# Kernel tuning notes

Hardware: AMD Instinct MI355X
Metric: run time of the kernel (lower is better)

The kernel has to match this reference:

```python
import jax, jax.numpy as jnp
import numpy as np
from jax import lax

NUM_CLASSES = 80
CONF_THRE = 0.01   # testconf in source
NMS_THRE = 0.2     # nmsthresh in source
N = 8400           # YOLOX anchors at 640x640: 80^2+40^2+20^2
IMG = 640.0


def setup_inputs() -> dict:
    key = jax.random.key(0)
    pred = jax.random.uniform(key, (N, 5 + NUM_CLASSES), dtype=jnp.float32)
    # scale cx,cy,w,h to pixel units so boxes are realistic
    pred = pred.at[:, :4].multiply(IMG)
    return {"prediction": pred}


def _pairwise_iou(boxes):
    # boxes: [N,4] in x1,y1,x2,y2
    area = (boxes[:, 2] - boxes[:, 0]) * (boxes[:, 3] - boxes[:, 1])  # [N]
    lt = jnp.maximum(boxes[:, None, :2], boxes[None, :, :2])  # [N,N,2]
    rb = jnp.minimum(boxes[:, None, 2:], boxes[None, :, 2:])  # [N,N,2]
    wh = jnp.clip(rb - lt, 0.0)
    inter = wh[..., 0] * wh[..., 1]
    return inter / (area[:, None] + area[None, :] - inter + 1e-9)


def reference(prediction):
    # ---- box corner decode (cx,cy,w,h -> x1,y1,x2,y2) ----
    cx, cy, w, h = prediction[:, 0], prediction[:, 1], prediction[:, 2], prediction[:, 3]
    boxes = jnp.stack([cx - w / 2, cy - h / 2, cx + w / 2, cy + h / 2], axis=1)

    # ---- per-class max ----
    cls_scores = prediction[:, 5:5 + NUM_CLASSES]
    class_conf = jnp.max(cls_scores, axis=1, keepdims=True)            # [N,1]
    class_pred = jnp.argmax(cls_scores, axis=1).astype(prediction.dtype)[:, None]

    obj = prediction[:, 4]
    valid = obj >= CONF_THRE                                            # conf mask

    # detections = [x1,y1,x2,y2, obj_conf, class_conf, class_pred]  -> [N,7]
    det = jnp.concatenate([boxes, obj[:, None], class_conf, class_pred], axis=1)

    # ---- class-agnostic greedy NMS on obj score (fixed-shape version) ----
    scores = jnp.where(valid, obj, -1.0)
    order = jnp.argsort(-scores)
    det_s = det[order]
    boxes_s = boxes[order]
    valid_s = valid[order]

    iou = _pairwise_iou(boxes_s)  # [N,N] ~282MB, dominant traffic
    idx = jnp.arange(N)

    def step(keep, inp):
        i, row, v = inp
        alive = keep[i] & v                      # only a kept valid box suppresses
        supp = alive & (row > NMS_THRE) & (idx > i)
        return keep & ~supp, None

    keep0 = jnp.ones((N,), dtype=bool)
    keep, _ = lax.scan(step, keep0, (idx, iou, valid_s))
    keep = keep & valid_s

    # suppressed / below-conf rows are zeroed (torch returns a ragged subset;
    # here we return the score-sorted, mask-zeroed fixed-shape equivalent)
    out = det_s * keep[:, None].astype(det_s.dtype)
    return out
```

## Files before the change

### kernel.cpp

```cpp
#include <hip/hip_runtime.h>
#include <stdint.h>

#define N_BOX 8400
#define NCLS 80
#define PSTRIDE 85
#define NW 132
#define NTILE 8778
#define ZROWI N_BOX
#define CONF_T 0.01f
#define NMS_T 0.2f

typedef unsigned long long u64;

#define OFF_DET     0
#define OFF_DIAGT   0
#define OFF_SUP1    67584
#define OFF_SUP2    135168
#define OFF_SUP3    202752
#define OFF_KEYS    268800
#define OFF_DETS    336000
#define OFF_BOXESS  604800
#define OFF_MASK    739200
#define OFF_KEEPW   9610656
#define OFF_VCNT    9611712

__device__ __forceinline__ unsigned fmap_desc(float f) {
    unsigned u = __float_as_uint(f);
    unsigned m = (u & 0x80000000u) ? ~u : (u | 0x80000000u);
    return ~m;
}

__device__ __forceinline__ u64 readlane64(u64 v, int lane) {
    unsigned lo = (unsigned)__builtin_amdgcn_readlane((int)(unsigned)v, lane);
    unsigned hi = (unsigned)__builtin_amdgcn_readlane((int)(unsigned)(v >> 32), lane);
    return ((u64)hi << 32) | lo;
}

__device__ __forceinline__ u64 shfl_xor64(u64 v, int m) {
    int lo = __shfl_xor((int)(unsigned)v, m);
    int hi = __shfl_xor((int)(unsigned)(v >> 32), m);
    return ((u64)(unsigned)hi << 32) | (unsigned)lo;
}

__device__ __forceinline__ u64 bittranspose64(u64 x, int lane) {
    const u64 P0 = 0x5555555555555555ull, P1 = 0x3333333333333333ull,
              P2 = 0x0F0F0F0F0F0F0F0Full, P3 = 0x00FF00FF00FF00FFull,
              P4 = 0x0000FFFF0000FFFFull, P5 = 0x00000000FFFFFFFFull;
#define TSTEP(s, p) do {                                                 \
        u64 y = shfl_xor64(x, s);                                        \
        x = (lane & (s)) ? ((x & ~(p)) | ((y & ~(p)) >> (s)))            \
                         : ((x & (p))  | ((y & (p))  << (s)));           \
    } while (0)
    TSTEP(1, P0); TSTEP(2, P1); TSTEP(4, P2);
    TSTEP(8, P3); TSTEP(16, P4); TSTEP(32, P5);
#undef TSTEP
    return x;
}

__device__ __forceinline__ u64 wmask(int w, int V) {
    int nb = V - (w << 6);
    if (nb <= 0) return 0ull;
    if (nb >= 64) return ~0ull;
    return (1ull << nb) - 1ull;
}

__device__ __forceinline__ void step_barrier() {
    asm volatile("s_waitcnt lgkmcnt(0)" ::: "memory");
    __builtin_amdgcn_s_barrier();
    asm volatile("" ::: "memory");
}

__global__ __launch_bounds__(256) void prep_k(const float* __restrict__ pred,
                                              float* __restrict__ det,
                                              unsigned* __restrict__ keys,
                                              u64* __restrict__ mask) {
    if (blockIdx.x == 0 && threadIdx.x < NW)
        mask[(size_t)ZROWI * NW + threadIdx.x] = 0ull;
    int gt = blockIdx.x * 256 + threadIdx.x;
    int i = gt >> 2, q = gt & 3;
    if (i >= N_BOX) return;
    const float* p = pred + (size_t)i * PSTRIDE;
    int cbase = q * 20;
    float best = p[5 + cbase];
    int arg = cbase;
    for (int c = 1; c < 20; ++c) {
        float v = p[5 + cbase + c];
        if (v > best) { best = v; arg = cbase + c; }
    }
    for (int d = 1; d < 4; d <<= 1) {
        float ob = __shfl_xor(best, d);
        int   oa = __shfl_xor(arg, d);
        if (ob > best || (ob == best && oa < arg)) { best = ob; arg = oa; }
    }
    if (q == 0) {
        float cx = p[0], cy = p[1], w = p[2], h = p[3], obj = p[4];
        float hw = __fmul_rn(w, 0.5f), hh = __fmul_rn(h, 0.5f);
        float x1 = __fsub_rn(cx, hw), y1 = __fsub_rn(cy, hh);
        float x2 = __fadd_rn(cx, hw), y2 = __fadd_rn(cy, hh);
        bool valid = (obj >= CONF_T);
        float score = valid ? obj : -1.0f;
        keys[i] = fmap_desc(score);
        float4* dr = (float4*)(det + (size_t)i * 8);
        dr[0] = make_float4(x1, y1, x2, y2);
        dr[1] = make_float4(obj, best, (float)arg, 0.0f);
    }
}

__global__ __launch_bounds__(256) void rank_k(const unsigned* __restrict__ keys,
                                              const float* __restrict__ det,
                                              float4* __restrict__ det_s,
                                              float4* __restrict__ boxes_s,
                                              int* __restrict__ vcount) {
    int t = threadIdx.x;
    int i = blockIdx.x * 32 + (t & 31);
    int s = t >> 5;
    unsigned my = (i < N_BOX) ? keys[i] : 0xFFFFFFFFu;
    int cnt = 0, cv = 0;
    int j0 = s * 1056;
    int jend = (s == 7) ? N_BOX : (j0 + 1056);
    for (int j = j0; j < jend; j += 4) {
        uint4 k4 = *(const uint4*)(keys + j);
        cnt += (k4.x < my) + (k4.y < my) + (k4.z < my) + (k4.w < my);
        cnt += (k4.x == my && j     < i) + (k4.y == my && j + 1 < i)
             + (k4.z == my && j + 2 < i) + (k4.w == my && j + 3 < i);
        cv  += ((int)k4.x >= 0) + ((int)k4.y >= 0) + ((int)k4.z >= 0) + ((int)k4.w >= 0);
    }
    __shared__ int sc[256], sv[256];
    sc[t] = cnt; sv[t] = cv;
    __syncthreads();
    if (t < 32) {
        int r = sc[t] + sc[t + 32] + sc[t + 64] + sc[t + 96]
              + sc[t + 128] + sc[t + 160] + sc[t + 192] + sc[t + 224];
        if (i < N_BOX) {
            const float4* dr = (const float4*)(det + (size_t)i * 8);
            float4 b0 = dr[0], b1 = dr[1];
            det_s[(size_t)r * 2]     = b0;
            det_s[(size_t)r * 2 + 1] = b1;
            boxes_s[r] = b0;
        }
        if (blockIdx.x == 0 && t == 0) {
            *vcount = sv[0] + sv[32] + sv[64] + sv[96]
                    + sv[128] + sv[160] + sv[192] + sv[224];
        }
    }
}

__global__ __launch_bounds__(64) void mask_k(const float4* __restrict__ boxes_s,
                                             u64* __restrict__ mask,
                                             u64* __restrict__ diagT,
                                             u64* __restrict__ sup1,
                                             u64* __restrict__ sup2,
                                             u64* __restrict__ sup3) {
    int tt = blockIdx.x, lane = threadIdx.x;
    int rb = (int)((2.0f * NW + 1.0f
                    - sqrtf((2.0f * NW + 1.0f) * (2.0f * NW + 1.0f) - 8.0f * (float)tt)) * 0.5f);
    while (rb > 0 && rb * NW - rb * (rb - 1) / 2 > tt) rb--;
    while ((rb + 1) * NW - (rb + 1) * rb / 2 <= tt) rb++;
    int cb = rb + (tt - (rb * NW - rb * (rb - 1) / 2));

    __shared__ float4 cB[64];
    __shared__ float  cA[64];
    int c0 = cb * 64 + lane;
    float4 b = (c0 < N_BOX) ? boxes_s[c0] : make_float4(0.f, 0.f, 0.f, 0.f);
    cB[lane] = b;
    cA[lane] = __fmul_rn(__fsub_rn(b.z, b.x), __fsub_rn(b.w, b.y));
    __syncthreads();
    int r = rb * 64 + lane;
    bool inb = (r < N_BOX);
    float4 rx = boxes_s[inb ? r : (N_BOX - 1)];
    float ra = __fmul_rn(__fsub_rn(rx.z, rx.x), __fsub_rn(rx.w, rx.y));
    u64 bits = 0ull;
    int cbase = cb * 64;
    for (int j = 0; j < 64; ++j) {
        int c = cbase + j;
        if (c >= N_BOX || c <= r) continue;
        float4 cx4 = cB[j];
        float ltx = fmaxf(rx.x, cx4.x), lty = fmaxf(rx.y, cx4.y);
        float rbx = fminf(rx.z, cx4.z), rby = fminf(rx.w, cx4.w);
        float wx = fmaxf(__fsub_rn(rbx, ltx), 0.0f);
        float wy = fmaxf(__fsub_rn(rby, lty), 0.0f);
        float inter = __fmul_rn(wx, wy);
        float denom = __fadd_rn(__fsub_rn(__fadd_rn(ra, cA[j]), inter), 1e-9f);
        float iou = __fdiv_rn(inter, denom);
        if (iou > NMS_T) bits |= (1ull << j);
    }
    if (inb) mask[(size_t)r * NW + cb] = bits;
    int d = cb - rb;
    if (d <= 3) {
        u64 tb = bittranspose64(bits, lane);
        size_t idx = (size_t)cb * 64 + lane;
        if (d == 0)      diagT[idx] = tb;
        else if (d == 1) sup1[idx]  = tb;
        else if (d == 2) sup2[idx]  = tb;
        else             sup3[idx]  = tb;
    }
}

__global__ __launch_bounds__(192, 1) void scan_k(const u64* __restrict__ mask,
                                                 const u64* __restrict__ diagT,
                                                 const u64* __restrict__ sup1,
                                                 const u64* __restrict__ sup2,
                                                 const u64* __restrict__ sup3,
                                                 const int* __restrict__ vcount,
                                                 u64* __restrict__ keepw) {
    __shared__ u64 remvP1[NW + 2];
    __shared__ u64 remvP2[NW + 2];
    __shared__ u64 Lbuf[NW];
    int tid = threadIdx.x, lane = tid & 63, wv = tid >> 6;
    int V = *vcount;
    for (int i = tid; i < NW + 2; i += 192) { remvP1[i] = 0ull; remvP2[i] = 0ull; }
    __syncthreads();

    if (wv == 0) {
        u64 A1 = 0ull, A2 = 0ull, A3 = 0ull;
        u64 d0P, s1P, s2P, s3P, d0Q, s1Q, s2Q, s3Q;
#define TL(S, kk) do {                                                   \
        int t_ = (kk) < NW ? (kk) : (NW - 1);                            \
        size_t ix_ = (size_t)t_ * 64 + lane;                             \
        d0##S = diagT[ix_]; s1##S = sup1[ix_];                           \
        s2##S = sup2[ix_];  s3##S = sup3[ix_];                           \
    } while (0)
#define STEP0(kk, S) do {                                                \
        int k_ = (kk);                                                   \
        u64 cur_ = remvP1[k_] | remvP2[k_];                              \
        cur_ |= __ballot((s1##S & A1) != 0ull);                          \
        cur_ |= __ballot((s2##S & A2) != 0ull);                          \
        cur_ |= __ballot((s3##S & A3) != 0ull);                          \
        u64 m_ = wmask(k_, V);                                           \
        u64 ns_ = (~cur_) & m_;                                          \
        u64 L_ = 0ull;                                                   \
        while (ns_) {                                                    \
            int b_ = __builtin_ctzll(ns_);                               \
            L_ |= 1ull << b_;                                            \
            u64 sup_ = __ballot((int)((d0##S >> b_) & 1ull));            \
            ns_ &= ~sup_;                                                \
            ns_ &= ~(1ull << b_);                                        \
        }                                                                \
        if (lane == 0) { Lbuf[k_] = L_; keepw[k_] = L_; }                \
        A3 = A2; A2 = A1; A1 = L_;                                       \
        TL(S, k_ + 2);                                                   \
        step_barrier();                                                  \
    } while (0)
        TL(P, 0);
        TL(Q, 1);
        for (int c = 0; c < NW; c += 2) {
            STEP0(c + 0, P);
            STEP0(c + 1, Q);
        }
#undef STEP0
#undef TL
    } else {
        int half = wv - 1;
        u64* myP = half ? remvP2 : remvP1;
        int tw = (lane < 4) ? (128 + lane) : 131;
        u64 Ra = 0ull, Rb = 0ull, Rc = 0ull;
        u64 Pa0=0,Pa1=0,Pa2=0,Pa3=0, Pb0=0,Pb1=0,Pb2=0,Pb3=0, Pc0=0,Pc1=0,Pc2=0,Pc3=0;
        u64 Qa0=0,Qa1=0,Qa2=0,Qa3=0, Qb0=0,Qb1=0,Qb2=0,Qb3=0, Qc0=0,Qc1=0,Qc2=0,Qc3=0;

#define CONS(S) do {                                                     \
        Ra |= (S##a0 | S##a1) | (S##a2 | S##a3);                         \
        Rb |= (S##b0 | S##b1) | (S##b2 | S##b3);                         \
        Rc |= (S##c0 | S##c1) | (S##c2 | S##c3);                         \
    } while (0)

#define LROW(S, i) do {                                                  \
        size_t ri_ = rem_ ? (size_t)(rbase_ + __builtin_ctz(rem_))       \
                          : (size_t)ZROWI;                               \
        rem_ &= rem_ - 1u;                                               \
        const u64* rp_ = mask + ri_ * NW;                                \
        ulonglong2 v_ = *(const ulonglong2*)(rp_ + 2 * lane);            \
        S##a##i = v_.x; S##b##i = v_.y; S##c##i = rp_[tw];               \
    } while (0)

#define STEP1(jj, S) do {                                                \
        int j_ = (jj);                                                   \
        CONS(S);                                  \
        int w_ = j_ + 1;                                                 \
        u64 rw_ = (w_ < 128) ? ((w_ & 1) ? Rb : Ra) : Rc;                \
        int sl_ = (w_ < 128) ? (w_ >> 1) : (w_ - 128);                   \
        u64 pv_ = readlane64(rw_, sl_);                                  \
        if (lane == 0) myP[w_] = pv_;                                    \
        u64 Lfull_ = (j_ >= 1) ? Lbuf[j_ - 1] : 0ull;                    \
        unsigned rem_ = half ? (unsigned)(Lfull_ >> 32)                  \
                             : (unsigned)Lfull_;                         \
        int rbase_ = ((j_ - 1) << 6) + 32 * half;                        \
        LROW(S, 0); LROW(S, 1); LROW(S, 2); LROW(S, 3);                  \
        while (rem_) {                              \
            u64 xa_ = 0, xb_ = 0, xc_ = 0;                               \
            for (int q_ = 0; q_ < 8; ++q_) {                             \
                size_t ri_ = rem_ ? (size_t)(rbase_ + __builtin_ctz(rem_)) \
                                  : (size_t)ZROWI;                       \
                rem_ &= rem_ - 1u;                                       \
                const u64* rp_ = mask + ri_ * NW;                        \
                ulonglong2 v_ = *(const ulonglong2*)(rp_ + 2 * lane);    \
                xa_ |= v_.x; xb_ |= v_.y; xc_ |= rp_[tw];                \
            }                                                            \
            Ra |= xa_; Rb |= xb_; Rc |= xc_;                             \
        }                                                                \
        step_barrier();                                                  \
    } while (0)

        for (int c = 0; c < NW; c += 2) {
            STEP1(c + 0, P);
            STEP1(c + 1, Q);
        }
#undef STEP1
#undef LROW
#undef CONS
    }
}

__global__ __launch_bounds__(256) void out_k(const float* __restrict__ det_s,
                                             const u64* __restrict__ keepw,
                                             float* __restrict__ out) {
    int e = blockIdx.x * 256 + threadIdx.x;
    if (e >= N_BOX * 7) return;
    int r = e / 7, c = e - r * 7;
    bool k = (keepw[r >> 6] >> (r & 63)) & 1ull;
    out[e] = k ? det_s[r * 8 + c] : 0.0f;
}

extern "C" void kernel_launch(void* const* d_in, const int* in_sizes, int n_in,
                              void* d_out, int out_size, void* d_ws, size_t ws_size,
                              hipStream_t stream) {
    const float* pred = (const float*)d_in[0];
    char* ws = (char*)d_ws;
    float*    det     = (float*)   (ws + OFF_DET);
    u64*      diagT   = (u64*)     (ws + OFF_DIAGT);
    u64*      sup1    = (u64*)     (ws + OFF_SUP1);
    u64*      sup2    = (u64*)     (ws + OFF_SUP2);
    u64*      sup3    = (u64*)     (ws + OFF_SUP3);
    unsigned* keys    = (unsigned*)(ws + OFF_KEYS);
    float*    det_s   = (float*)   (ws + OFF_DETS);
    float4*   boxes_s = (float4*)  (ws + OFF_BOXESS);
    u64*      mask    = (u64*)     (ws + OFF_MASK);
    u64*      keepw   = (u64*)     (ws + OFF_KEEPW);
    int*      vcount  = (int*)     (ws + OFF_VCNT);

    prep_k<<<132, 256, 0, stream>>>(pred, det, keys, mask);
    rank_k<<<264, 256, 0, stream>>>(keys, det, (float4*)det_s, boxes_s, vcount);
    mask_k<<<NTILE, 64, 0, stream>>>(boxes_s, mask, diagT, sup1, sup2, sup3);
    scan_k<<<1, 192, 0, stream>>>(mask, diagT, sup1, sup2, sup3, vcount, keepw);
    out_k <<<(N_BOX * 7 + 255) / 256, 256, 0, stream>>>(det_s, keepw, (float*)d_out);
}
```

Baseline: 155.0 us.

## Fuse output write into scan, pack index into sort keys, batch mask tiles

The output-zeroing kernel is folded into the single-block scan kernel. It now reads the keep bits from shared memory instead of a global keepw buffer, which saves one launch and a global round trip. Sort keys become 64-bit, with the original index packed in the low bits, so the rank kernel no longer needs a separate tie-break comparison. The mask kernel now processes four 64x64 tiles per 256-thread block instead of one tile per 64-thread block. The risk is that the fused output loop runs on only 192 threads of a single block, which serialises about 58.8k stores that were previously spread across many blocks.

```diff
diff --git a/kernel.cpp b/kernel.cpp
--- a/kernel.cpp
+++ b/kernel.cpp
@@ -21,7 +21,6 @@
 #define OFF_DETS    336000
 #define OFF_BOXESS  604800
 #define OFF_MASK    739200
-#define OFF_KEEPW   9610656
 #define OFF_VCNT    9611712
 
 __device__ __forceinline__ unsigned fmap_desc(float f) {
@@ -72,7 +71,7 @@
 
 __global__ __launch_bounds__(256) void prep_k(const float* __restrict__ pred,
                                               float* __restrict__ det,
-                                              unsigned* __restrict__ keys,
+                                              u64* __restrict__ keys,
                                               u64* __restrict__ mask) {
     if (blockIdx.x == 0 && threadIdx.x < NW)
         mask[(size_t)ZROWI * NW + threadIdx.x] = 0ull;
@@ -99,14 +98,14 @@
         float x2 = __fadd_rn(cx, hw), y2 = __fadd_rn(cy, hh);
         bool valid = (obj >= CONF_T);
         float score = valid ? obj : -1.0f;
-        keys[i] = fmap_desc(score);
+        keys[i] = ((u64)fmap_desc(score) << 32) | (unsigned)i;
         float4* dr = (float4*)(det + (size_t)i * 8);
         dr[0] = make_float4(x1, y1, x2, y2);
         dr[1] = make_float4(obj, best, (float)arg, 0.0f);
     }
 }
 
-__global__ __launch_bounds__(256) void rank_k(const unsigned* __restrict__ keys,
+__global__ __launch_bounds__(256) void rank_k(const u64* __restrict__ keys,
                                               const float* __restrict__ det,
                                               float4* __restrict__ det_s,
                                               float4* __restrict__ boxes_s,
@@ -114,16 +113,13 @@
     int t = threadIdx.x;
     int i = blockIdx.x * 32 + (t & 31);
     int s = t >> 5;
-    unsigned my = (i < N_BOX) ? keys[i] : 0xFFFFFFFFu;
+    u64 my = (i < N_BOX) ? keys[i] : ~0ull;
     int cnt = 0, cv = 0;
-    int j0 = s * 1056;
-    int jend = (s == 7) ? N_BOX : (j0 + 1056);
-    for (int j = j0; j < jend; j += 4) {
-        uint4 k4 = *(const uint4*)(keys + j);
-        cnt += (k4.x < my) + (k4.y < my) + (k4.z < my) + (k4.w < my);
-        cnt += (k4.x == my && j     < i) + (k4.y == my && j + 1 < i)
-             + (k4.z == my && j + 2 < i) + (k4.w == my && j + 3 < i);
-        cv  += ((int)k4.x >= 0) + ((int)k4.y >= 0) + ((int)k4.z >= 0) + ((int)k4.w >= 0);
+    int j0 = s * 1050, j1 = j0 + 1050;
+    for (int j = j0; j < j1; j += 2) {
+        ulonglong2 kk = *(const ulonglong2*)(keys + j);
+        cnt += (kk.x < my) + (kk.y < my);
+        cv  += ((long long)kk.x >= 0) + ((long long)kk.y >= 0);
     }
     __shared__ int sc[256], sv[256];
     sc[t] = cnt; sv[t] = cv;
@@ -145,26 +141,31 @@
     }
 }
 
-__global__ __launch_bounds__(64) void mask_k(const float4* __restrict__ boxes_s,
-                                             u64* __restrict__ mask,
-                                             u64* __restrict__ diagT,
-                                             u64* __restrict__ sup1,
-                                             u64* __restrict__ sup2,
-                                             u64* __restrict__ sup3) {
-    int tt = blockIdx.x, lane = threadIdx.x;
-    int rb = (int)((2.0f * NW + 1.0f
+__global__ __launch_bounds__(256) void mask_k(const float4* __restrict__ boxes_s,
+                                              u64* __restrict__ mask,
+                                              u64* __restrict__ diagT,
+                                              u64* __restrict__ sup1,
+                                              u64* __restrict__ sup2,
+                                              u64* __restrict__ sup3) {
+    int sub = threadIdx.x >> 6, lane = threadIdx.x & 63;
+    int tt = blockIdx.x * 4 + sub;
+    bool tv = (tt < NTILE);
+    __shared__ float4 cB[4][64];
+    __shared__ float  cA[4][64];
+    int rb = 0, cb = 0;
+    if (tv) {
+        rb = (int)((2.0f * NW + 1.0f
                     - sqrtf((2.0f * NW + 1.0f) * (2.0f * NW + 1.0f) - 8.0f * (float)tt)) * 0.5f);
-    while (rb > 0 && rb * NW - rb * (rb - 1) / 2 > tt) rb--;
-    while ((rb + 1) * NW - (rb + 1) * rb / 2 <= tt) rb++;
-    int cb = rb + (tt - (rb * NW - rb * (rb - 1) / 2));
-
-    __shared__ float4 cB[64];
-    __shared__ float  cA[64];
-    int c0 = cb * 64 + lane;
-    float4 b = (c0 < N_BOX) ? boxes_s[c0] : make_float4(0.f, 0.f, 0.f, 0.f);
-    cB[lane] = b;
-    cA[lane] = __fmul_rn(__fsub_rn(b.z, b.x), __fsub_rn(b.w, b.y));
+        while (rb > 0 && rb * NW - rb * (rb - 1) / 2 > tt) rb--;
+        while ((rb + 1) * NW - (rb + 1) * rb / 2 <= tt) rb++;
+        cb = rb + (tt - (rb * NW - rb * (rb - 1) / 2));
+        int c0 = cb * 64 + lane;
+        float4 b = (c0 < N_BOX) ? boxes_s[c0] : make_float4(0.f, 0.f, 0.f, 0.f);
+        cB[sub][lane] = b;
+        cA[sub][lane] = __fmul_rn(__fsub_rn(b.z, b.x), __fsub_rn(b.w, b.y));
+    }
     __syncthreads();
+    if (!tv) return;
     int r = rb * 64 + lane;
     bool inb = (r < N_BOX);
     float4 rx = boxes_s[inb ? r : (N_BOX - 1)];
@@ -174,13 +175,13 @@
     for (int j = 0; j < 64; ++j) {
         int c = cbase + j;
         if (c >= N_BOX || c <= r) continue;
-        float4 cx4 = cB[j];
+        float4 cx4 = cB[sub][j];
         float ltx = fmaxf(rx.x, cx4.x), lty = fmaxf(rx.y, cx4.y);
         float rbx = fminf(rx.z, cx4.z), rby = fminf(rx.w, cx4.w);
         float wx = fmaxf(__fsub_rn(rbx, ltx), 0.0f);
         float wy = fmaxf(__fsub_rn(rby, lty), 0.0f);
         float inter = __fmul_rn(wx, wy);
-        float denom = __fadd_rn(__fsub_rn(__fadd_rn(ra, cA[j]), inter), 1e-9f);
+        float denom = __fadd_rn(__fsub_rn(__fadd_rn(ra, cA[sub][j]), inter), 1e-9f);
         float iou = __fdiv_rn(inter, denom);
         if (iou > NMS_T) bits |= (1ull << j);
     }
@@ -202,7 +203,8 @@
                                                  const u64* __restrict__ sup2,
                                                  const u64* __restrict__ sup3,
                                                  const int* __restrict__ vcount,
-                                                 u64* __restrict__ keepw) {
+                                                 const float* __restrict__ det_s,
+                                                 float* __restrict__ out) {
     __shared__ u64 remvP1[NW + 2];
     __shared__ u64 remvP2[NW + 2];
     __shared__ u64 Lbuf[NW];
@@ -236,7 +238,7 @@
             ns_ &= ~sup_;                                                \
             ns_ &= ~(1ull << b_);                                        \
         }                                                                \
-        if (lane == 0) { Lbuf[k_] = L_; keepw[k_] = L_; }                \
+        if (lane == 0) Lbuf[k_] = L_;                                    \
         A3 = A2; A2 = A1; A1 = L_;                                       \
         TL(S, k_ + 2);                                                   \
         step_barrier();                                                  \
@@ -308,16 +310,13 @@
 #undef LROW
 #undef CONS
     }
-}
-
-__global__ __launch_bounds__(256) void out_k(const float* __restrict__ det_s,
-                                             const u64* __restrict__ keepw,
-                                             float* __restrict__ out) {
-    int e = blockIdx.x * 256 + threadIdx.x;
-    if (e >= N_BOX * 7) return;
-    int r = e / 7, c = e - r * 7;
-    bool k = (keepw[r >> 6] >> (r & 63)) & 1ull;
-    out[e] = k ? det_s[r * 8 + c] : 0.0f;
+
+    __syncthreads();
+    for (int e = tid; e < N_BOX * 7; e += 192) {
+        int r = e / 7, c = e - r * 7;
+        bool k = (Lbuf[r >> 6] >> (r & 63)) & 1ull;
+        out[e] = k ? det_s[(size_t)r * 8 + c] : 0.0f;
+    }
 }
 
 extern "C" void kernel_launch(void* const* d_in, const int* in_sizes, int n_in,
@@ -330,16 +329,15 @@
     u64*      sup1    = (u64*)     (ws + OFF_SUP1);
     u64*      sup2    = (u64*)     (ws + OFF_SUP2);
     u64*      sup3    = (u64*)     (ws + OFF_SUP3);
-    unsigned* keys    = (unsigned*)(ws + OFF_KEYS);
+    u64*      keys    = (u64*)     (ws + OFF_KEYS);
     float*    det_s   = (float*)   (ws + OFF_DETS);
     float4*   boxes_s = (float4*)  (ws + OFF_BOXESS);
     u64*      mask    = (u64*)     (ws + OFF_MASK);
-    u64*      keepw   = (u64*)     (ws + OFF_KEEPW);
     int*      vcount  = (int*)     (ws + OFF_VCNT);
 
     prep_k<<<132, 256, 0, stream>>>(pred, det, keys, mask);
     rank_k<<<264, 256, 0, stream>>>(keys, det, (float4*)det_s, boxes_s, vcount);
-    mask_k<<<NTILE, 64, 0, stream>>>(boxes_s, mask, diagT, sup1, sup2, sup3);
-    scan_k<<<1, 192, 0, stream>>>(mask, diagT, sup1, sup2, sup3, vcount, keepw);
-    out_k <<<(N_BOX * 7 + 255) / 256, 256, 0, stream>>>(det_s, keepw, (float*)d_out);
-}
+    mask_k<<<(NTILE + 3) / 4, 256, 0, stream>>>(boxes_s, mask, diagT, sup1, sup2, sup3);
+    scan_k<<<1, 192, 0, stream>>>(mask, diagT, sup1, sup2, sup3, vcount,
+                                  det_s, (float*)d_out);
+}
```

Result: slower. 202.7 us (+30.8%).
